# Performance work log

Hardware: AMD Instinct MI355X
Metric: run time of the kernel (lower is better)

The kernel has to match this reference:

```python
import jax, jax.numpy as jnp
import numpy as np

B, T, DIN, DOUT, G = 8, 4096, 1024, 1024, 16
S = T // G  # equal-length contiguous segments


def setup_inputs() -> dict:
    key = jax.random.key(0)
    k1, k2, k3 = jax.random.split(key, 3)
    x = jax.random.normal(k1, (B, T, DIN), dtype=jnp.float32)
    # Embedding(num_groups, dim_in*dim_out) viewed as (dim_out, dim_in) per group
    W = jax.random.normal(k2, (G, DOUT, DIN), dtype=jnp.float32) * (1.0 / np.sqrt(DIN))
    b = jax.random.normal(k3, (G, DOUT), dtype=jnp.float32) * 0.02
    # sorted, contiguous, equal-length segments: [0,...,0,1,...,1,...,G-1]
    indices = jnp.repeat(jnp.arange(G, dtype=jnp.int64), S)
    return {"x": x, "W": W, "b": b, "indices": indices, "num_groups": G}


def reference(x, W, b, indices, num_groups):
    # SegmentLinear: for each contiguous segment of `indices`, apply the
    # group's linear layer out[:, sl] = x[:, sl] @ W[g].T + b[g].
    # With equal-length contiguous segments this is one grouped GEMM.
    Bc, Tc, Din = x.shape
    g = num_groups
    s = Tc // g
    xg = x.reshape(Bc, g, s, Din)                      # [B, G, S, din]
    out = jnp.einsum('bgsd,god->bgso', xg, W)          # grouped GEMM
    out = out + b[None, :, None, :]                    # per-group bias
    return out.reshape(Bc, Tc, -1)
```

## Files before the change

### kernel.cpp

```cpp
#include <hip/hip_runtime.h>

#define B_    8
#define T_    4096
#define DIN_  1024
#define DOUT_ 1024
#define G_    16
#define S_    256

#define BM 256
#define BN 256
#define BK 64
#define NKT (DIN_ / BK)
#define HALF_E 8192

#define NX (B_ * T_ * DIN_)
#define NW (G_ * DOUT_ * DIN_)
#define WS_NEEDED ((size_t)(NX + NW) * 2)

typedef __bf16 bf16x8 __attribute__((ext_vector_type(8)));
typedef float  f32x4  __attribute__((ext_vector_type(4)));

__device__ __forceinline__ void gload_lds16(const void* g, void* l) {
    __builtin_amdgcn_global_load_lds(
        (const __attribute__((address_space(1))) unsigned int*)g,
        (__attribute__((address_space(3))) unsigned int*)l,
        16 , 0, 0);
}

__global__ __launch_bounds__(256)
void cvt_f32_bf16_2(const float* __restrict__ inX, __bf16* __restrict__ outX, int nx8,
                    const float* __restrict__ inW, __bf16* __restrict__ outW, int nw8) {
    const int total = nx8 + nw8;
    int i = blockIdx.x * 256 + threadIdx.x;
    const int stride = gridDim.x * 256;
    for (; i < total; i += stride) {
        const float* in;
        __bf16* out;
        long k;
        if (i < nx8) { in = inX; out = outX; k = (long)i * 8; }
        else         { in = inW; out = outW; k = (long)(i - nx8) * 8; }
        const f32x4 a = *(const f32x4*)(in + k);
        const f32x4 b = *(const f32x4*)(in + k + 4);
        bf16x8 h;
        #pragma unroll
        for (int u = 0; u < 4; ++u) { h[u] = (__bf16)a[u]; h[u + 4] = (__bf16)b[u]; }
        *(bf16x8*)(out + k) = h;
    }
}

__global__ __launch_bounds__(512, 2)
void seg_gemm_bf16(const __bf16* __restrict__ Xb, const __bf16* __restrict__ Wb,
                   const float* __restrict__ Bias, float* __restrict__ Out)
{
    __shared__ __attribute__((aligned(16))) __bf16 As[4 * HALF_E];
    __shared__ __attribute__((aligned(16))) __bf16 Bs[4 * HALF_E];

    const int raw = blockIdx.x;
    const int bid = ((raw & 7) << 6) | (raw >> 3);
    const int g   = bid >> 5;
    const int mT  = (bid >> 2) & 7;
    const int nT  = bid & 3;

    const int tid  = threadIdx.x;
    const int lane = tid & 63;
    const int w    = tid >> 6;
    const int wm   = w >> 2;
    const int wn   = w & 3;

    const long rowBase = (long)mT * T_ + (long)g * S_;
    const long colBase = (long)g * DOUT_ + (long)nT * BN;

    const int srow = w * 16 + (lane >> 2);
    const int scol = ((lane & 3) ^ ((lane >> 4) & 3)) * 8;
    const __bf16* gA = Xb + (rowBase + srow) * DIN_ + scol;
    const __bf16* gB = Wb + (colBase + srow) * DIN_ + scol;
    const int dOff = w * 512 + lane * 8;

    const int ml  = lane & 15;
    const int h   = lane >> 4;
    const int hx8 = (h ^ ((ml >> 2) & 3)) * 8;

    f32x4 acc[8][4] = {};

#define HA(T, KH) (As + ((((T) & 1) << 1) + (KH)) * HALF_E)
#define HB(T, KH) (Bs + ((((T) & 1) << 1) + (KH)) * HALF_E)
#define STG_A(T, KH) do {                                                  \
    const __bf16* p_ = gA + (T) * BK + (KH) * 32;                          \
    gload_lds16(p_,              HA(T, KH) + dOff);                        \
    gload_lds16(p_ + 128 * DIN_, HA(T, KH) + dOff + 4096);                 \
} while (0)
#define STG_B(T, KH) do {                                                  \
    const __bf16* p_ = gB + (T) * BK + (KH) * 32;                          \
    gload_lds16(p_,              HB(T, KH) + dOff);                        \
    gload_lds16(p_ + 128 * DIN_, HB(T, KH) + dOff + 4096);                 \
} while (0)

#define VMW(N)  asm volatile("s_waitcnt vmcnt(" #N ")" ::: "memory")
#define NOPV    ((void)0)

#define PH(T, KH, ILO, NEWB, STAGE, VM, ENDBAR) do {                       \
    const __bf16* Ah_ = HA(T, KH);                                         \
    if (NEWB) {                                                            \
        const __bf16* Bh_ = HB(T, KH);                                     \
        _Pragma("unroll")                                                  \
        for (int j_ = 0; j_ < 4; ++j_)                                     \
            bF[j_] = *(const bf16x8*)&Bh_[(wn * 64 + j_ * 16 + ml) * 32 + hx8]; \
    }                                                                      \
    _Pragma("unroll")                                                      \
    for (int i_ = 0; i_ < 4; ++i_)                                         \
        aF[i_] = *(const bf16x8*)&Ah_[(wm * 128 + ((ILO) + i_) * 16 + ml) * 32 + hx8]; \
    STAGE;                                                                 \
    asm volatile("" ::: "memory");                                         \
    __builtin_amdgcn_s_barrier();                                          \
    asm volatile("s_waitcnt lgkmcnt(0)" ::: "memory");                     \
    __builtin_amdgcn_sched_barrier(0);                                     \
    __builtin_amdgcn_s_setprio(1);                                         \
    _Pragma("unroll")                                                      \
    for (int i_ = 0; i_ < 4; ++i_)                                         \
        _Pragma("unroll")                                                  \
        for (int j_ = 0; j_ < 4; ++j_)                                     \
            acc[(ILO) + i_][j_] = __builtin_amdgcn_mfma_f32_16x16x32_bf16( \
                aF[i_], bF[j_], acc[(ILO) + i_][j_], 0, 0, 0);             \
    __builtin_amdgcn_s_setprio(0);                                         \
    VM;                                                                    \
    if (ENDBAR) {                                                          \
        asm volatile("" ::: "memory");                                     \
        __builtin_amdgcn_s_barrier();                                      \
        asm volatile("" ::: "memory");                                     \
    }                                                                      \
} while (0)

#define TILE(T, DS01, DS23, VM, LAST) do {                                 \
    bf16x8 aF[4], bF[4];                                                   \
    PH(T, 0, 0, true,  if (DS01) STG_A((T) + 1, 1), NOPV, true);           \
    PH(T, 0, 4, false, if (DS01) STG_B((T) + 1, 1), NOPV, true);           \
    PH(T, 1, 0, true,  if (DS23) STG_A((T) + 2, 0), NOPV, true);           \
    PH(T, 1, 4, false, if (DS23) STG_B((T) + 2, 0), VM, !(LAST));          \
} while (0)

    STG_A(0, 0); STG_B(0, 0); STG_A(0, 1); STG_B(0, 1);
    STG_A(1, 0); STG_B(1, 0);
    VMW(4);
    __builtin_amdgcn_s_barrier();
    asm volatile("" ::: "memory");

    for (int T = 0; T < 14; T += 2) {
        TILE(T,     true, true, VMW(4), false);
        TILE(T + 1, true, true, VMW(4), false);
    }
    TILE(14, true,  false, VMW(0), false);
    TILE(15, false, false, NOPV,   true);

    const int ncolBase = nT * BN + wn * 64;
    #pragma unroll
    for (int j = 0; j < 4; ++j) {
        const int n = ncolBase + j * 16 + ml;
        const float bj = Bias[g * DOUT_ + n];
        #pragma unroll
        for (int i = 0; i < 8; ++i) {
            const long row0 = rowBase + wm * 128 + i * 16 + h * 4;
            #pragma unroll
            for (int r = 0; r < 4; ++r)
                Out[(row0 + r) * DOUT_ + n] = acc[i][j][r] + bj;
        }
    }
#undef TILE
#undef PH
#undef STG_A
#undef STG_B
#undef HA
#undef HB
}

#define FBM 128
#define FBN 128
#define LDKF 40
__global__ __launch_bounds__(256, 2)
void seg_linear_fused(const float* __restrict__ X, const float* __restrict__ W,
                      const float* __restrict__ Bias, float* __restrict__ Out)
{
    __shared__ __attribute__((aligned(16))) __bf16 Asf[FBM * LDKF];
    __shared__ __attribute__((aligned(16))) __bf16 Bsf[FBN * LDKF];

    const int bid = blockIdx.x;
    const int g   = bid >> 7;
    const int rb  = bid & 127;
    const int mT  = rb >> 3;
    const int nT  = rb & 7;

    const int tid  = threadIdx.x;
    const int lane = tid & 63;
    const int wid  = tid >> 6;
    const int wr   = wid >> 1;
    const int wc   = wid & 1;

    const long rowBase = (long)(mT >> 1) * T_ + (long)g * S_ + (mT & 1) * FBM;

    const float* Abase = X + rowBase * DIN_;
    const float* Bbase = W + ((long)g * DOUT_ + (long)nT * FBN) * DIN_;

    const int srow = tid >> 1;
    const int scol = (tid & 1) * 16;
    const float* pA = Abase + (long)srow * DIN_ + scol;
    const float* pB = Bbase + (long)srow * DIN_ + scol;
    __bf16* wA = &Asf[srow * LDKF + scol];
    __bf16* wB = &Bsf[srow * LDKF + scol];

    f32x4 acc[4][4] = {};
    const int q8 = (lane >> 4) * 8;
    const int ml = lane & 15;

    for (int k0 = 0; k0 < DIN_; k0 += 32) {
        f32x4 va0 = *(const f32x4*)(pA + k0);
        f32x4 va1 = *(const f32x4*)(pA + k0 + 4);
        f32x4 va2 = *(const f32x4*)(pA + k0 + 8);
        f32x4 va3 = *(const f32x4*)(pA + k0 + 12);
        f32x4 vb0 = *(const f32x4*)(pB + k0);
        f32x4 vb1 = *(const f32x4*)(pB + k0 + 4);
        f32x4 vb2 = *(const f32x4*)(pB + k0 + 8);
        f32x4 vb3 = *(const f32x4*)(pB + k0 + 12);

        bf16x8 ha0, ha1, hb0, hb1;
        #pragma unroll
        for (int u = 0; u < 4; ++u) {
            ha0[u] = (__bf16)va0[u]; ha0[u + 4] = (__bf16)va1[u];
            ha1[u] = (__bf16)va2[u]; ha1[u + 4] = (__bf16)va3[u];
            hb0[u] = (__bf16)vb0[u]; hb0[u + 4] = (__bf16)vb1[u];
            hb1[u] = (__bf16)vb2[u]; hb1[u + 4] = (__bf16)vb3[u];
        }
        *(bf16x8*)(wA) = ha0; *(bf16x8*)(wA + 8) = ha1;
        *(bf16x8*)(wB) = hb0; *(bf16x8*)(wB + 8) = hb1;

        __syncthreads();

        bf16x8 aF[4], bF[4];
        #pragma unroll
        for (int i = 0; i < 4; ++i)
            aF[i] = *(const bf16x8*)&Asf[(wr * 64 + i * 16 + ml) * LDKF + q8];
        #pragma unroll
        for (int j = 0; j < 4; ++j)
            bF[j] = *(const bf16x8*)&Bsf[(wc * 64 + j * 16 + ml) * LDKF + q8];
        #pragma unroll
        for (int i = 0; i < 4; ++i)
            #pragma unroll
            for (int j = 0; j < 4; ++j)
                acc[i][j] = __builtin_amdgcn_mfma_f32_16x16x32_bf16(aF[i], bF[j], acc[i][j], 0, 0, 0);
        __syncthreads();
    }

    const int mq = lane >> 4;
    const int ncol = nT * FBN + wc * 64;
    #pragma unroll
    for (int j = 0; j < 4; ++j) {
        const int n = ncol + j * 16 + ml;
        const float bj = Bias[g * DOUT_ + n];
        #pragma unroll
        for (int i = 0; i < 4; ++i) {
            const long row0 = rowBase + wr * 64 + i * 16 + mq * 4;
            #pragma unroll
            for (int r = 0; r < 4; ++r)
                Out[(row0 + r) * DOUT_ + n] = acc[i][j][r] + bj;
        }
    }
}

extern "C" void kernel_launch(void* const* d_in, const int* in_sizes, int n_in,
                              void* d_out, int out_size, void* d_ws, size_t ws_size,
                              hipStream_t stream) {
    const float* X    = (const float*)d_in[0];
    const float* W    = (const float*)d_in[1];
    const float* Bias = (const float*)d_in[2];
    float* Out = (float*)d_out;

    if (ws_size >= WS_NEEDED) {
        __bf16* Xb = (__bf16*)d_ws;
        __bf16* Wb = Xb + NX;
        cvt_f32_bf16_2<<<dim3(2048), dim3(256), 0, stream>>>(X, Xb, NX / 8, W, Wb, NW / 8);
        const int grid = G_ * (B_ * S_ / BM) * (DOUT_ / BN);
        seg_gemm_bf16<<<dim3(grid), dim3(512), 0, stream>>>(Xb, Wb, Bias, Out);
    } else {
        const int grid = G_ * (B_ * S_ / FBM) * (DOUT_ / FBN);
        seg_linear_fused<<<dim3(grid), dim3(256), 0, stream>>>(X, W, Bias, Out);
    }
}
```

Measured before the change: 155.9 us.

## Switch GEMM LDS staging to full-BK tiles with double buffering

```diff
diff --git a/kernel.cpp b/kernel.cpp
--- a/kernel.cpp
+++ b/kernel.cpp
@@ -11,7 +11,7 @@
 #define BN 256
 #define BK 64
 #define NKT (DIN_ / BK)
-#define HALF_E 8192
+#define TILE_E (BM * BK)
 
 #define NX (B_ * T_ * DIN_)
 #define NW (G_ * DOUT_ * DIN_)
@@ -52,8 +52,8 @@
 void seg_gemm_bf16(const __bf16* __restrict__ Xb, const __bf16* __restrict__ Wb,
                    const float* __restrict__ Bias, float* __restrict__ Out)
 {
-    __shared__ __attribute__((aligned(16))) __bf16 As[4 * HALF_E];
-    __shared__ __attribute__((aligned(16))) __bf16 Bs[4 * HALF_E];
+    __shared__ __attribute__((aligned(16))) __bf16 As[2 * TILE_E];
+    __shared__ __attribute__((aligned(16))) __bf16 Bs[2 * TILE_E];
 
     const int raw = blockIdx.x;
     const int bid = ((raw & 7) << 6) | (raw >> 3);
@@ -70,45 +70,43 @@
     const long rowBase = (long)mT * T_ + (long)g * S_;
     const long colBase = (long)g * DOUT_ + (long)nT * BN;
 
-    const int srow = w * 16 + (lane >> 2);
-    const int scol = ((lane & 3) ^ ((lane >> 4) & 3)) * 8;
-    const __bf16* gA = Xb + (rowBase + srow) * DIN_ + scol;
-    const __bf16* gB = Wb + (colBase + srow) * DIN_ + scol;
-    const int dOff = w * 512 + lane * 8;
+    const int srow = w * 8 + (lane >> 3);
+    const int scol = ((lane & 7) ^ (lane >> 3)) * 8;
+    const __bf16* srcA = Xb + (rowBase + srow) * DIN_ + scol;
+    const __bf16* srcB = Wb + (colBase + srow) * DIN_ + scol;
+    const int w512 = w * 512;
 
     const int ml  = lane & 15;
     const int h   = lane >> 4;
-    const int hx8 = (h ^ ((ml >> 2) & 3)) * 8;
+    const int sp0 = ((0 + h) ^ (ml & 7)) * 8;
+    const int sp1 = ((4 + h) ^ (ml & 7)) * 8;
 
     f32x4 acc[8][4] = {};
-
-#define HA(T, KH) (As + ((((T) & 1) << 1) + (KH)) * HALF_E)
-#define HB(T, KH) (Bs + ((((T) & 1) << 1) + (KH)) * HALF_E)
-#define STG_A(T, KH) do {                                                  \
-    const __bf16* p_ = gA + (T) * BK + (KH) * 32;                          \
-    gload_lds16(p_,              HA(T, KH) + dOff);                        \
-    gload_lds16(p_ + 128 * DIN_, HA(T, KH) + dOff + 4096);                 \
-} while (0)
-#define STG_B(T, KH) do {                                                  \
-    const __bf16* p_ = gB + (T) * BK + (KH) * 32;                          \
-    gload_lds16(p_,              HB(T, KH) + dOff);                        \
-    gload_lds16(p_ + 128 * DIN_, HB(T, KH) + dOff + 4096);                 \
-} while (0)
 
 #define VMW(N)  asm volatile("s_waitcnt vmcnt(" #N ")" ::: "memory")
 #define NOPV    ((void)0)
 
-#define PH(T, KH, ILO, NEWB, STAGE, VM, ENDBAR) do {                       \
-    const __bf16* Ah_ = HA(T, KH);                                         \
+#define STG(T, H) do {                                                     \
+    const long ko_ = (long)(T) * BK;                                       \
+    __bf16* dA_ = As + ((T) & 1) * TILE_E + (H) * 8192 + w512;             \
+    __bf16* dB_ = Bs + ((T) & 1) * TILE_E + (H) * 8192 + w512;             \
+    gload_lds16(srcA + ((H) * 128)      * DIN_ + ko_, dA_);                \
+    gload_lds16(srcA + ((H) * 128 + 64) * DIN_ + ko_, dA_ + 4096);         \
+    gload_lds16(srcB + ((H) * 128)      * DIN_ + ko_, dB_);                \
+    gload_lds16(srcB + ((H) * 128 + 64) * DIN_ + ko_, dB_ + 4096);         \
+} while (0)
+
+#define PH(TT, SPOFF, ILO, NEWB, STAGE, DOVM, ENDBAR) do {                 \
+    const __bf16* Ab_ = As + ((TT) & 1) * TILE_E;                          \
     if (NEWB) {                                                            \
-        const __bf16* Bh_ = HB(T, KH);                                     \
+        const __bf16* Bb_ = Bs + ((TT) & 1) * TILE_E;                      \
         _Pragma("unroll")                                                  \
         for (int j_ = 0; j_ < 4; ++j_)                                     \
-            bF[j_] = *(const bf16x8*)&Bh_[(wn * 64 + j_ * 16 + ml) * 32 + hx8]; \
+            bF[j_] = *(const bf16x8*)&Bb_[(wn * 64 + j_ * 16 + ml) * BK + (SPOFF)]; \
     }                                                                      \
     _Pragma("unroll")                                                      \
     for (int i_ = 0; i_ < 4; ++i_)                                         \
-        aF[i_] = *(const bf16x8*)&Ah_[(wm * 128 + ((ILO) + i_) * 16 + ml) * 32 + hx8]; \
+        aF[i_] = *(const bf16x8*)&Ab_[(wm * 128 + ((ILO) + i_) * 16 + ml) * BK + (SPOFF)]; \
     STAGE;                                                                 \
     asm volatile("" ::: "memory");                                         \
     __builtin_amdgcn_s_barrier();                                          \
@@ -122,7 +120,7 @@
             acc[(ILO) + i_][j_] = __builtin_amdgcn_mfma_f32_16x16x32_bf16( \
                 aF[i_], bF[j_], acc[(ILO) + i_][j_], 0, 0, 0);             \
     __builtin_amdgcn_s_setprio(0);                                         \
-    VM;                                                                    \
+    if (DOVM) VMW(0);                                                      \
     if (ENDBAR) {                                                          \
         asm volatile("" ::: "memory");                                     \
         __builtin_amdgcn_s_barrier();                                      \
@@ -130,26 +128,22 @@
     }                                                                      \
 } while (0)
 
-#define TILE(T, DS01, DS23, VM, LAST) do {                                 \
+#define TILE(T, DOSTG, DOVM, FINAL) do {                                   \
     bf16x8 aF[4], bF[4];                                                   \
-    PH(T, 0, 0, true,  if (DS01) STG_A((T) + 1, 1), NOPV, true);           \
-    PH(T, 0, 4, false, if (DS01) STG_B((T) + 1, 1), NOPV, true);           \
-    PH(T, 1, 0, true,  if (DS23) STG_A((T) + 2, 0), NOPV, true);           \
-    PH(T, 1, 4, false, if (DS23) STG_B((T) + 2, 0), VM, !(LAST));          \
+    PH(T, sp0, 0, true,  if (DOSTG) STG((T) + 1, 0), false, true);         \
+    PH(T, sp0, 4, false, if (DOSTG) STG((T) + 1, 1), false, true);         \
+    PH(T, sp1, 0, true,  NOPV,                       false, true);         \
+    PH(T, sp1, 4, false, NOPV,                       DOVM, !(FINAL));      \
 } while (0)
 
-    STG_A(0, 0); STG_B(0, 0); STG_A(0, 1); STG_B(0, 1);
-    STG_A(1, 0); STG_B(1, 0);
-    VMW(4);
+    STG(0, 0); STG(0, 1);
+    VMW(0);
     __builtin_amdgcn_s_barrier();
     asm volatile("" ::: "memory");
 
-    for (int T = 0; T < 14; T += 2) {
-        TILE(T,     true, true, VMW(4), false);
-        TILE(T + 1, true, true, VMW(4), false);
-    }
-    TILE(14, true,  false, VMW(0), false);
-    TILE(15, false, false, NOPV,   true);
+    for (int t = 0; t < NKT - 1; ++t)
+        TILE(t, true, true, false);
+    TILE(15, false, false, true);
 
     const int ncolBase = nT * BN + wn * 64;
     #pragma unroll
@@ -166,10 +160,7 @@
     }
 #undef TILE
 #undef PH
-#undef STG_A
-#undef STG_B
-#undef HA
-#undef HB
+#undef STG
 }
 
 #define FBM 128
```

Result: no change. 157.6 us (+1.1%).
